# Kernel optimization log

Hardware: AMD Instinct MI355X
Metric: run time of the kernel (lower is better)

Reference implementation:

```python
import jax, jax.numpy as jnp
import numpy as np
import math

S, B, D, H = 2048, 4, 1024, 16
DH = D // H

def setup_inputs() -> dict:
    key = jax.random.key(0)
    ks = jax.random.split(key, 6)
    x = jax.random.normal(ks[0], (S, B, D), dtype=jnp.float32)
    # causal additive mask (finite large negative for numerical safety)
    i = jnp.arange(S)
    attn_mask = jnp.where(i[None, :] > i[:, None], jnp.float32(-1e9), jnp.float32(0.0))
    beta = jnp.zeros((H,), dtype=jnp.float32)  # per-head log-scale, init 0 -> exp=1
    xav = math.sqrt(6.0 / (D + D))  # xavier_uniform bound
    Wq = jax.random.uniform(ks[1], (D, D), minval=-xav, maxval=xav, dtype=jnp.float32)
    Wk = jax.random.uniform(ks[2], (D, D), minval=-xav, maxval=xav, dtype=jnp.float32)
    Wv = jax.random.uniform(ks[3], (D, D), minval=-xav, maxval=xav, dtype=jnp.float32)
    Wo = jax.random.uniform(ks[4], (D, D), minval=-xav, maxval=xav, dtype=jnp.float32)
    z = jnp.zeros((D,), dtype=jnp.float32)
    return {"x": x, "attn_mask": attn_mask, "beta": beta,
            "Wq": Wq, "bq": z, "Wk": Wk, "bk": z, "Wv": Wv, "bv": z, "Wo": Wo, "bo": z}

def reference(x, attn_mask, beta, Wq, bq, Wk, bk, Wv, bv, Wo, bo):
    s, b, d = x.shape
    h, dh = H, DH
    q = x @ Wq.T + bq  # (s, b, d)
    k = x @ Wk.T + bk
    v = x @ Wv.T + bv
    # attn_sink: append zero key/value token, pad mask with a zero column
    k = jnp.concatenate([k, jnp.zeros((1, b, d), k.dtype)], axis=0)  # (s+1, b, d)
    v = jnp.concatenate([v, jnp.zeros((1, b, d), v.dtype)], axis=0)
    mask = jnp.pad(attn_mask, ((0, 0), (0, 1)))  # (s, s+1)
    t = s + 1
    # split heads: (seq, b, h, dh) -> (b, h, seq, dh)
    qh = q.reshape(s, b, h, dh).transpose(1, 2, 0, 3)
    kh = k.reshape(t, b, h, dh).transpose(1, 2, 0, 3)
    vh = v.reshape(t, b, h, dh).transpose(1, 2, 0, 3)
    scale = (jnp.exp(beta) * math.sqrt(dh))[None, :, None, None]
    qh = qh / scale
    scores = jnp.einsum('bhsd,bhtd->bhst', qh, kh) + mask[None, None]
    w = jax.nn.softmax(scores, axis=-1)
    out = jnp.einsum('bhst,bhtd->bhsd', w, vh)  # (b, h, s, dh)
    out = out.transpose(2, 0, 1, 3).reshape(s, b, d)
    return out @ Wo.T + bo
```

## Files before the change

### kernel.cpp

```cpp
#include <hip/hip_runtime.h>
#include <hip/hip_bf16.h>
#include <math.h>

#define S_LEN   2048
#define BATCH   4
#define DMODEL  1024
#define NHEAD   16
#define DHEAD   64
#define MROWS   (S_LEN * BATCH)

typedef __bf16 bf16;
typedef __bf16 bf16x8 __attribute__((ext_vector_type(8)));
typedef __bf16 bf16x4 __attribute__((ext_vector_type(4)));
typedef short  short4_t __attribute__((ext_vector_type(4)));
typedef float  f32x4  __attribute__((ext_vector_type(4)));

#define LOG2E 1.4426950408889634f

#define AS1C(p) (const __attribute__((address_space(1))) void*)(p)
#define AS3(p)  (__attribute__((address_space(3))) void*)(p)


__global__ __launch_bounds__(256) void cast_bf16(const float* __restrict__ in,
                                                 bf16* __restrict__ out, int n8) {
    int i = blockIdx.x * 256 + threadIdx.x;
    if (i >= n8) return;
    const float4* p = (const float4*)in;
    float4 a = p[i * 2], b = p[i * 2 + 1];
    bf16x8 o;
    o[0] = (bf16)a.x; o[1] = (bf16)a.y; o[2] = (bf16)a.z; o[3] = (bf16)a.w;
    o[4] = (bf16)b.x; o[5] = (bf16)b.y; o[6] = (bf16)b.z; o[7] = (bf16)b.w;
    *(bf16x8*)(out + (size_t)i * 8) = o;
}

__global__ __launch_bounds__(256) void cast3_bf16(const float* __restrict__ w0,
                                                  const float* __restrict__ w1,
                                                  const float* __restrict__ w2,
                                                  bf16* __restrict__ out) {
    const int seg = blockIdx.y;
    const float* in = (seg == 0) ? w0 : (seg == 1) ? w1 : w2;
    int i = blockIdx.x * 256 + threadIdx.x;
    const float4* p = (const float4*)in;
    float4 a = p[i * 2], b = p[i * 2 + 1];
    bf16x8 o;
    o[0] = (bf16)a.x; o[1] = (bf16)a.y; o[2] = (bf16)a.z; o[3] = (bf16)a.w;
    o[4] = (bf16)b.x; o[5] = (bf16)b.y; o[6] = (bf16)b.z; o[7] = (bf16)b.w;
    *(bf16x8*)(out + (size_t)seg * DMODEL * DMODEL + (size_t)i * 8) = o;
}

__global__ __launch_bounds__(512, 4) void qkv_gemm(const bf16* __restrict__ A,
                                                   const bf16* __restrict__ W,
                                                   const float* __restrict__ bq,
                                                   const float* __restrict__ bk,
                                                   const float* __restrict__ bv,
                                                   const float* __restrict__ beta,
                                                   bf16* __restrict__ Qo,
                                                   bf16* __restrict__ Kp,
                                                   bf16* __restrict__ Vp) {
    constexpr int BK = 32;
    constexpr int NT = DMODEL / BK;
    __shared__ __align__(16) bf16 sA[3][256 * BK];
    __shared__ __align__(16) bf16 sB[3][128 * BK];
    const int t    = threadIdx.x;
    const int lane = t & 63;
    const int wave = t >> 6;
    const int wr   = wave >> 2;
    const int wc   = wave & 3;
    const int lq   = lane & 15;
    const int lg   = lane >> 4;
    const int bn   = blockIdx.x * 128;
    const int bm   = blockIdx.y * 256;

    const int schunk = (lane & 3) ^ ((lane >> 3) & 3);
    const bf16* ApS  = A + (size_t)(bm + wave * 32 + (lane >> 2)) * DMODEL + schunk * 8;
    const bf16* ApS2 = ApS + (size_t)16 * DMODEL;
    const bf16* WpS  = W + (size_t)(bn + wave * 16 + (lane >> 2)) * DMODEL + schunk * 8;
    const int koff = (lg ^ ((lq >> 1) & 3)) * 8;
    f32x4 acc[8][2] = {};

    __builtin_amdgcn_global_load_lds(AS1C(ApS),       AS3(&sA[0][wave*1024]),       16,0,0);
    __builtin_amdgcn_global_load_lds(AS1C(ApS2),      AS3(&sA[0][wave*1024 + 512]), 16,0,0);
    __builtin_amdgcn_global_load_lds(AS1C(WpS),       AS3(&sB[0][wave*512]),        16,0,0);
    __builtin_amdgcn_global_load_lds(AS1C(ApS  + BK), AS3(&sA[1][wave*1024]),       16,0,0);
    __builtin_amdgcn_global_load_lds(AS1C(ApS2 + BK), AS3(&sA[1][wave*1024 + 512]), 16,0,0);
    __builtin_amdgcn_global_load_lds(AS1C(WpS  + BK), AS3(&sB[1][wave*512]),        16,0,0);
    asm volatile("s_waitcnt vmcnt(3)\n\ts_barrier" ::: "memory");

    int bi = 0, si = 2, st = 2;
    for (int tt = 0; tt < NT; ++tt) {
        {
            const size_t ko = (size_t)st * BK;
            __builtin_amdgcn_global_load_lds(AS1C(ApS  + ko), AS3(&sA[si][wave*1024]),       16,0,0);
            __builtin_amdgcn_global_load_lds(AS1C(ApS2 + ko), AS3(&sA[si][wave*1024 + 512]), 16,0,0);
            __builtin_amdgcn_global_load_lds(AS1C(WpS  + ko), AS3(&sB[si][wave*512]),        16,0,0);
        }
        const bf16* At = sA[bi];
        const bf16* Bt = sB[bi];
        bf16x8 bf0 = *(const bf16x8*)&Bt[(wc*32 +      lq)*BK + koff];
        bf16x8 bf1 = *(const bf16x8*)&Bt[(wc*32 + 16 + lq)*BK + koff];
        bf16x8 af0[4];
#pragma unroll
        for (int mt = 0; mt < 4; mt++)
            af0[mt] = *(const bf16x8*)&At[(wr*128 + mt*16 + lq)*BK + koff];
        __builtin_amdgcn_s_setprio(1);
#pragma unroll
        for (int mt = 0; mt < 4; mt++) {
            acc[mt][0] = __builtin_amdgcn_mfma_f32_16x16x32_bf16(af0[mt], bf0, acc[mt][0],0,0,0);
            acc[mt][1] = __builtin_amdgcn_mfma_f32_16x16x32_bf16(af0[mt], bf1, acc[mt][1],0,0,0);
        }
        __builtin_amdgcn_s_setprio(0);
        bf16x8 af1[4];
#pragma unroll
        for (int mt = 0; mt < 4; mt++)
            af1[mt] = *(const bf16x8*)&At[(wr*128 + (mt+4)*16 + lq)*BK + koff];
        __builtin_amdgcn_s_setprio(1);
#pragma unroll
        for (int mt = 0; mt < 4; mt++) {
            acc[mt+4][0] = __builtin_amdgcn_mfma_f32_16x16x32_bf16(af1[mt], bf0, acc[mt+4][0],0,0,0);
            acc[mt+4][1] = __builtin_amdgcn_mfma_f32_16x16x32_bf16(af1[mt], bf1, acc[mt+4][1],0,0,0);
        }
        __builtin_amdgcn_s_setprio(0);
        asm volatile("s_waitcnt vmcnt(3)\n\ts_barrier" ::: "memory");
        bi = (bi == 2) ? 0 : bi + 1;
        si = (si == 2) ? 0 : si + 1;
        st = (st == NT - 1) ? 0 : st + 1;
    }

    const int seg = blockIdx.x >> 3;
    const int bnl = (blockIdx.x & 7) * 128;
    const float* bias = (seg == 0) ? bq : (seg == 1) ? bk : bv;

    if (seg == 0) {
#pragma unroll
        for (int nt = 0; nt < 2; nt++) {
            const int col = bnl + wc * 32 + nt * 16 + lq;
            const float bvv = bias[col];
            const float sc = LOG2E / (__expf(beta[col >> 6]) * 8.0f);
#pragma unroll
            for (int mt = 0; mt < 8; mt++) {
                const int row = bm + wr * 128 + mt * 16 + lg * 4;
#pragma unroll
                for (int r = 0; r < 4; r++) {
                    float v = (acc[mt][nt][r] + bvv) * sc;
                    Qo[(size_t)(row + r) * DMODEL + col] = (bf16)v;
                }
            }
        }
    } else {
        bf16* out = (seg == 1) ? Kp : Vp;
#pragma unroll
        for (int mt = 0; mt < 8; mt++) {
            const int F   = bm + wr * 128 + mt * 16;
            const int S0X = F >> 2;
            const int T   = S0X >> 4;
            const int sl  = (S0X & 15) + lg;
#pragma unroll
            for (int nt = 0; nt < 2; nt++) {
                const int col = bnl + wc * 32 + nt * 16 + lq;
                const int h   = col >> 6;
                const int dh  = col & 63;
                const float bvv = bias[col];
#pragma unroll
                for (int r = 0; r < 4; r++) {
                    float v = acc[mt][nt][r] + bvv;
                    size_t addr;
                    if (seg == 1) {
                        addr = ((size_t)((r * 16 + h) * 128 + T)) * 1024
                             + (dh >> 5) * 512
                             + (sl + 16 * ((dh >> 3) & 3)) * 8
                             + (dh & 7);
                    } else {
                        addr = ((size_t)((r * 16 + h) * 128 + T)) * 1024
                             + (dh >> 4) * 256 + ((dh & 15) + 16 * (sl >> 2)) * 4
                             + (sl & 3);
                    }
                    out[addr] = (bf16)v;
                }
            }
        }
    }
}

__global__ __launch_bounds__(256, 3) void gemm_out(const bf16* __restrict__ A,
                                                   const bf16* __restrict__ W,
                                                   const float* __restrict__ bias,
                                                   float* __restrict__ C) {
    constexpr int BK = 32;
    constexpr int NTILES = DMODEL / BK;
    __shared__ __align__(16) bf16 sA[3][128 * BK];
    __shared__ __align__(16) bf16 sB[3][128 * BK];

    const int t    = threadIdx.x;
    const int lane = t & 63;
    const int wave = t >> 6;
    const int wr   = wave >> 1;
    const int wc   = wave & 1;
    const int lq   = lane & 15;
    const int lg   = lane >> 4;
    const int bn   = blockIdx.x * 128;
    const int bm   = blockIdx.y * 128;

    const int schunk = (lane & 3) ^ ((lane >> 3) & 3);
    const bf16* ApS = A + (size_t)(bm + wave * 32 + (lane >> 2)) * DMODEL + schunk * 8;
    const bf16* WpS = W + (size_t)(bn + wave * 32 + (lane >> 2)) * DMODEL + schunk * 8;
    const int koff = (lg ^ ((lq >> 1) & 3)) * 8;

    f32x4 acc[4][4] = {};

#define OSTAGE(si_, ko_)                                                                              \
    __builtin_amdgcn_global_load_lds(AS1C(ApS + (ko_)),               AS3(&sA[si_][(wave*32 +  0)*BK]), 16,0,0); \
    __builtin_amdgcn_global_load_lds(AS1C(ApS + 16*DMODEL + (ko_)),   AS3(&sA[si_][(wave*32 + 16)*BK]), 16,0,0); \
    __builtin_amdgcn_global_load_lds(AS1C(WpS + (ko_)),               AS3(&sB[si_][(wave*32 +  0)*BK]), 16,0,0); \
    __builtin_amdgcn_global_load_lds(AS1C(WpS + 16*DMODEL + (ko_)),   AS3(&sB[si_][(wave*32 + 16)*BK]), 16,0,0);

    OSTAGE(0, 0)
    OSTAGE(1, BK)
    asm volatile("s_waitcnt vmcnt(4)\n\ts_barrier" ::: "memory");

    int bi = 0, si = 2, st = 2;
    for (int tt = 0; tt < NTILES; ++tt) {
        OSTAGE(si, (size_t)st * BK)
        const bf16* At = sA[bi];
        const bf16* Bt = sB[bi];
        bf16x8 bfr[4], af[4];
#pragma unroll
        for (int nt = 0; nt < 4; nt++)
            bfr[nt] = *(const bf16x8*)&Bt[(wc * 64 + nt * 16 + lq) * BK + koff];
#pragma unroll
        for (int mt = 0; mt < 4; mt++)
            af[mt] = *(const bf16x8*)&At[(wr * 64 + mt * 16 + lq) * BK + koff];
        __builtin_amdgcn_s_setprio(1);
#pragma unroll
        for (int mt = 0; mt < 4; mt++)
#pragma unroll
            for (int nt = 0; nt < 4; nt++)
                acc[mt][nt] = __builtin_amdgcn_mfma_f32_16x16x32_bf16(af[mt], bfr[nt], acc[mt][nt], 0, 0, 0);
        __builtin_amdgcn_s_setprio(0);
        asm volatile("s_waitcnt vmcnt(4)\n\ts_barrier" ::: "memory");
        bi = (bi == 2) ? 0 : bi + 1;
        si = (si == 2) ? 0 : si + 1;
        st = (st == NTILES - 1) ? 0 : st + 1;
    }
#undef OSTAGE

#pragma unroll
    for (int nt = 0; nt < 4; nt++) {
        const int col = bn + wc * 64 + nt * 16 + lq;
        const float bvv = bias[col];
#pragma unroll
        for (int mt = 0; mt < 4; mt++) {
            const int row = bm + wr * 64 + mt * 16 + lg * 4;
#pragma unroll
            for (int r = 0; r < 4; r++)
                C[(size_t)(row + r) * DMODEL + col] = acc[mt][nt][r] + bvv;
        }
    }
}

__global__ __launch_bounds__(256, 3) void attn_kernel(const bf16* __restrict__ Q,
                                                      const bf16* __restrict__ Kp,
                                                      const bf16* __restrict__ Vp,
                                                      bf16* __restrict__ O) {
    __shared__ __align__(16) float sO[64 * 65];
    __shared__ __align__(16) float sL[256];

    const int t    = threadIdx.x;
    const int lane = t & 63;
    const int wave = t >> 6;
    const int lq = lane & 15;
    const int lg = lane >> 4;

    const int bid = (int)blockIdx.x + 32 * ((int)blockIdx.y + 16 * (int)blockIdx.z);
    const int swz = (bid & 7) * 256 + (bid >> 3);
    const int qi  = 31 - (swz & 31);
    const int h   = (swz >> 5) & 15;
    const int b   = swz >> 9;
    const int qb  = qi * 64;

    bf16x8 qf[4][2];
#pragma unroll
    for (int nt = 0; nt < 4; nt++)
#pragma unroll
        for (int kc = 0; kc < 2; kc++)
            qf[nt][kc] = *(const bf16x8*)
                &Q[((size_t)(qb + nt * 16 + lq) * BATCH + b) * DMODEL + h * DHEAD + kc * 32 + lg * 8];

    f32x4 o_acc[4][4] = {};
    float l_lane[4] = {0.f, 0.f, 0.f, 0.f};

    const bf16* Kb = Kp + (size_t)(b * NHEAD + h) * 131072;
    const bf16* Vb = Vp + (size_t)(b * NHEAD + h) * 131072;

    bf16x8 kc0 = *(const bf16x8*)(Kb + (size_t)wave * 1024 + lane * 8);
    bf16x8 kc1 = *(const bf16x8*)(Kb + (size_t)wave * 1024 + 512 + lane * 8);
    bf16x4 vc0 = *(const bf16x4*)(Vb + (size_t)wave * 1024 +   0 + lane * 4);
    bf16x4 vc1 = *(const bf16x4*)(Vb + (size_t)wave * 1024 + 256 + lane * 4);
    bf16x4 vc2 = *(const bf16x4*)(Vb + (size_t)wave * 1024 + 512 + lane * 4);
    bf16x4 vc3 = *(const bf16x4*)(Vb + (size_t)wave * 1024 + 768 + lane * 4);

    for (int kt = 0; kt <= qi; kt++) {
        const int tn = ((kt < qi) ? (kt + 1) : 0) * 4 + wave;
        const bf16* Kn = Kb + (size_t)tn * 1024;
        const bf16* Vn = Vb + (size_t)tn * 1024;
        bf16x8 kn0 = *(const bf16x8*)(Kn + lane * 8);
        bf16x8 kn1 = *(const bf16x8*)(Kn + 512 + lane * 8);
        bf16x4 vn0 = *(const bf16x4*)(Vn +   0 + lane * 4);
        bf16x4 vn1 = *(const bf16x4*)(Vn + 256 + lane * 4);
        bf16x4 vn2 = *(const bf16x4*)(Vn + 512 + lane * 4);
        bf16x4 vn3 = *(const bf16x4*)(Vn + 768 + lane * 4);

        f32x4 st[4];
        __builtin_amdgcn_s_setprio(1);
#pragma unroll
        for (int nt = 0; nt < 4; nt++) {
            f32x4 a = {};
            a = __builtin_amdgcn_mfma_f32_16x16x32_bf16(kc0, qf[nt][0], a, 0, 0, 0);
            a = __builtin_amdgcn_mfma_f32_16x16x32_bf16(kc1, qf[nt][1], a, 0, 0, 0);
            st[nt] = a;
        }
        __builtin_amdgcn_s_setprio(0);

        if (kt == qi) {
#pragma unroll
            for (int nt = 0; nt < 4; nt++)
#pragma unroll
                for (int r = 0; r < 4; r++)
                    if (wave * 16 + lg * 4 + r > nt * 16 + lq) st[nt][r] = -1e30f;
        }

        short4_t pf[4];
#pragma unroll
        for (int nt = 0; nt < 4; nt++) {
            float p0 = __builtin_amdgcn_exp2f(st[nt][0]);
            float p1 = __builtin_amdgcn_exp2f(st[nt][1]);
            float p2 = __builtin_amdgcn_exp2f(st[nt][2]);
            float p3 = __builtin_amdgcn_exp2f(st[nt][3]);
            l_lane[nt] += (p0 + p1) + (p2 + p3);
            bf16x4 pv;
            pv[0] = (bf16)p0; pv[1] = (bf16)p1; pv[2] = (bf16)p2; pv[3] = (bf16)p3;
            pf[nt] = __builtin_bit_cast(short4_t, pv);
        }

        short4_t va0 = __builtin_bit_cast(short4_t, vc0);
        short4_t va1 = __builtin_bit_cast(short4_t, vc1);
        short4_t va2 = __builtin_bit_cast(short4_t, vc2);
        short4_t va3 = __builtin_bit_cast(short4_t, vc3);
        __builtin_amdgcn_s_setprio(1);
#pragma unroll
        for (int nt = 0; nt < 4; nt++) {
            o_acc[0][nt] = __builtin_amdgcn_mfma_f32_16x16x16bf16_1k(va0, pf[nt], o_acc[0][nt], 0, 0, 0);
            o_acc[1][nt] = __builtin_amdgcn_mfma_f32_16x16x16bf16_1k(va1, pf[nt], o_acc[1][nt], 0, 0, 0);
            o_acc[2][nt] = __builtin_amdgcn_mfma_f32_16x16x16bf16_1k(va2, pf[nt], o_acc[2][nt], 0, 0, 0);
            o_acc[3][nt] = __builtin_amdgcn_mfma_f32_16x16x16bf16_1k(va3, pf[nt], o_acc[3][nt], 0, 0, 0);
        }
        __builtin_amdgcn_s_setprio(0);

        kc0 = kn0; kc1 = kn1;
        vc0 = vn0; vc1 = vn1; vc2 = vn2; vc3 = vn3;
    }

#pragma unroll
    for (int nt = 0; nt < 4; nt++) {
        float v = l_lane[nt];
        v += __shfl_xor(v, 16);
        v += __shfl_xor(v, 32);
        if (lg == 0) sL[wave * 64 + nt * 16 + lq] = v;
    }

#pragma unroll
    for (int rd = 0; rd < 4; rd++) {
#pragma unroll
        for (int dtc = 0; dtc < 4; dtc++) {
            if (((wave + rd) & 3) == dtc) {
                if (rd == 0) {
#pragma unroll
                    for (int nt = 0; nt < 4; nt++)
#pragma unroll
                        for (int r = 0; r < 4; r++)
                            sO[(dtc * 16 + lg * 4 + r) * 65 + nt * 16 + lq] = o_acc[dtc][nt][r];
                } else {
#pragma unroll
                    for (int nt = 0; nt < 4; nt++)
#pragma unroll
                        for (int r = 0; r < 4; r++)
                            sO[(dtc * 16 + lg * 4 + r) * 65 + nt * 16 + lq] += o_acc[dtc][nt][r];
                }
            }
        }
        __syncthreads();
    }

    const int dt = wave;
    float rec[4];
#pragma unroll
    for (int nt = 0; nt < 4; nt++) {
        float lt = 1.0f + sL[nt * 16 + lq] + sL[64 + nt * 16 + lq]
                 + sL[128 + nt * 16 + lq] + sL[192 + nt * 16 + lq];
        rec[nt] = 1.0f / lt;
    }
#pragma unroll
    for (int nt = 0; nt < 4; nt++) {
        bf16x4 ov;
#pragma unroll
        for (int r = 0; r < 4; r++)
            ov[r] = (bf16)(sO[(dt * 16 + lg * 4 + r) * 65 + nt * 16 + lq] * rec[nt]);
        *(bf16x4*)&O[((size_t)(qb + nt * 16 + lq) * BATCH + b) * DMODEL + h * DHEAD + dt * 16 + lg * 4] = ov;
    }
}

extern "C" void kernel_launch(void* const* d_in, const int* in_sizes, int n_in,
                              void* d_out, int out_size, void* d_ws, size_t ws_size,
                              hipStream_t stream) {
    const float* x    = (const float*)d_in[0];
    const float* beta = (const float*)d_in[2];
    const float* Wq   = (const float*)d_in[3];
    const float* bq   = (const float*)d_in[4];
    const float* Wk   = (const float*)d_in[5];
    const float* bk   = (const float*)d_in[6];
    const float* Wv   = (const float*)d_in[7];
    const float* bv   = (const float*)d_in[8];
    const float* Wo   = (const float*)d_in[9];
    const float* bo   = (const float*)d_in[10];
    float* out = (float*)d_out;

    char* ws = (char*)d_ws;
    size_t off = 0;
    auto alloc = [&](size_t bytes) -> void* {
        void* p = ws + off;
        off += (bytes + 255) & ~(size_t)255;
        return p;
    };
    const size_t xbytes = (size_t)MROWS * DMODEL * sizeof(bf16);
    const size_t wbytes = (size_t)DMODEL * DMODEL * sizeof(bf16);
    bf16* xb   = (bf16*)alloc(xbytes);
    bf16* wqkv = (bf16*)alloc(3 * wbytes);
    bf16* wob  = (bf16*)alloc(wbytes);
    bf16* qws  = (bf16*)alloc(xbytes);
    bf16* kpb  = (bf16*)alloc(xbytes);
    bf16* vpb  = (bf16*)alloc(xbytes);
    bf16* aob  = (bf16*)alloc(xbytes);

    const int nx8 = MROWS * DMODEL / 8;
    const int nw8 = DMODEL * DMODEL / 8;
    cast_bf16<<<(nx8 + 255) / 256, 256, 0, stream>>>(x, xb, nx8);
    cast_bf16<<<(nw8 + 255) / 256, 256, 0, stream>>>(Wo, wob, nw8);
    dim3 c3grid(nw8 / 256, 3);
    cast3_bf16<<<c3grid, 256, 0, stream>>>(Wq, Wk, Wv, wqkv);

    dim3 qgrid(3 * DMODEL / 128, MROWS / 256);
    qkv_gemm<<<qgrid, 512, 0, stream>>>(xb, wqkv, bq, bk, bv, beta, qws, kpb, vpb);

    dim3 agrid(S_LEN / 64, NHEAD, BATCH);
    attn_kernel<<<agrid, 256, 0, stream>>>(qws, kpb, vpb, aob);

    dim3 ogrid(DMODEL / 128, MROWS / 128);
    gemm_out<<<ogrid, 256, 0, stream>>>(aob, wob, bo, out);
}
```

Baseline: 281.7 us.

## Pair causal query tiles per attention block and merge cast kernels

The attention kernel now launches half as many blocks, and each block handles two query tiles (qi and 31-qi). Every block therefore does the same amount of causal work, which balances load and removes the tail from uneven block lengths. Separately, the three fp32-to-bf16 cast launches are folded into a single kernel that selects its source and destination by index. The risk is fewer, longer blocks with two serial passes, which could reduce overlap and occupancy.

```diff
diff --git a/kernel.cpp b/kernel.cpp
--- a/kernel.cpp
+++ b/kernel.cpp
@@ -21,31 +21,37 @@
 #define AS3(p)  (__attribute__((address_space(3))) void*)(p)
 
 
-__global__ __launch_bounds__(256) void cast_bf16(const float* __restrict__ in,
-                                                 bf16* __restrict__ out, int n8) {
-    int i = blockIdx.x * 256 + threadIdx.x;
-    if (i >= n8) return;
-    const float4* p = (const float4*)in;
-    float4 a = p[i * 2], b = p[i * 2 + 1];
+__global__ __launch_bounds__(256) void cast_all(const float* __restrict__ x,
+                                                const float* __restrict__ wq,
+                                                const float* __restrict__ wk,
+                                                const float* __restrict__ wv,
+                                                const float* __restrict__ wo,
+                                                bf16* __restrict__ xb,
+                                                bf16* __restrict__ wqkv,
+                                                bf16* __restrict__ wob) {
+    const int i = blockIdx.x * 256 + threadIdx.x;
+    constexpr int NX8 = MROWS * DMODEL / 8;
+    constexpr int NW8 = DMODEL * DMODEL / 8;
+    const float* src;
+    bf16* dst;
+    int k;
+    if (i < NX8) {
+        src = x; dst = xb; k = i;
+    } else {
+        const int j   = i - NX8;
+        const int seg = j >> 17;
+        k = j & (NW8 - 1);
+        if (seg == 0)      { src = wq; dst = wqkv; }
+        else if (seg == 1) { src = wk; dst = wqkv + (size_t)DMODEL * DMODEL; }
+        else if (seg == 2) { src = wv; dst = wqkv + (size_t)2 * DMODEL * DMODEL; }
+        else               { src = wo; dst = wob; }
+    }
+    const float4* p = (const float4*)src;
+    float4 a = p[(size_t)k * 2], b = p[(size_t)k * 2 + 1];
     bf16x8 o;
     o[0] = (bf16)a.x; o[1] = (bf16)a.y; o[2] = (bf16)a.z; o[3] = (bf16)a.w;
     o[4] = (bf16)b.x; o[5] = (bf16)b.y; o[6] = (bf16)b.z; o[7] = (bf16)b.w;
-    *(bf16x8*)(out + (size_t)i * 8) = o;
-}
-
-__global__ __launch_bounds__(256) void cast3_bf16(const float* __restrict__ w0,
-                                                  const float* __restrict__ w1,
-                                                  const float* __restrict__ w2,
-                                                  bf16* __restrict__ out) {
-    const int seg = blockIdx.y;
-    const float* in = (seg == 0) ? w0 : (seg == 1) ? w1 : w2;
-    int i = blockIdx.x * 256 + threadIdx.x;
-    const float4* p = (const float4*)in;
-    float4 a = p[i * 2], b = p[i * 2 + 1];
-    bf16x8 o;
-    o[0] = (bf16)a.x; o[1] = (bf16)a.y; o[2] = (bf16)a.z; o[3] = (bf16)a.w;
-    o[4] = (bf16)b.x; o[5] = (bf16)b.y; o[6] = (bf16)b.z; o[7] = (bf16)b.w;
-    *(bf16x8*)(out + (size_t)seg * DMODEL * DMODEL + (size_t)i * 8) = o;
+    *(bf16x8*)(dst + (size_t)k * 8) = o;
 }
 
 __global__ __launch_bounds__(512, 4) void qkv_gemm(const bf16* __restrict__ A,
@@ -270,141 +276,148 @@
     const int lq = lane & 15;
     const int lg = lane >> 4;
 
-    const int bid = (int)blockIdx.x + 32 * ((int)blockIdx.y + 16 * (int)blockIdx.z);
-    const int swz = (bid & 7) * 256 + (bid >> 3);
-    const int qi  = 31 - (swz & 31);
-    const int h   = (swz >> 5) & 15;
-    const int b   = swz >> 9;
-    const int qb  = qi * 64;
-
-    bf16x8 qf[4][2];
-#pragma unroll
-    for (int nt = 0; nt < 4; nt++)
-#pragma unroll
-        for (int kc = 0; kc < 2; kc++)
-            qf[nt][kc] = *(const bf16x8*)
-                &Q[((size_t)(qb + nt * 16 + lq) * BATCH + b) * DMODEL + h * DHEAD + kc * 32 + lg * 8];
-
-    f32x4 o_acc[4][4] = {};
-    float l_lane[4] = {0.f, 0.f, 0.f, 0.f};
+    const int bid = (int)blockIdx.x + 16 * ((int)blockIdx.y + 16 * (int)blockIdx.z);
+    const int swz = (bid & 7) * 128 + (bid >> 3);
+    const int idx = swz & 15;
+    const int h   = (swz >> 4) & 15;
+    const int b   = swz >> 8;
 
     const bf16* Kb = Kp + (size_t)(b * NHEAD + h) * 131072;
     const bf16* Vb = Vp + (size_t)(b * NHEAD + h) * 131072;
 
-    bf16x8 kc0 = *(const bf16x8*)(Kb + (size_t)wave * 1024 + lane * 8);
-    bf16x8 kc1 = *(const bf16x8*)(Kb + (size_t)wave * 1024 + 512 + lane * 8);
-    bf16x4 vc0 = *(const bf16x4*)(Vb + (size_t)wave * 1024 +   0 + lane * 4);
-    bf16x4 vc1 = *(const bf16x4*)(Vb + (size_t)wave * 1024 + 256 + lane * 4);
-    bf16x4 vc2 = *(const bf16x4*)(Vb + (size_t)wave * 1024 + 512 + lane * 4);
-    bf16x4 vc3 = *(const bf16x4*)(Vb + (size_t)wave * 1024 + 768 + lane * 4);
-
-    for (int kt = 0; kt <= qi; kt++) {
-        const int tn = ((kt < qi) ? (kt + 1) : 0) * 4 + wave;
-        const bf16* Kn = Kb + (size_t)tn * 1024;
-        const bf16* Vn = Vb + (size_t)tn * 1024;
-        bf16x8 kn0 = *(const bf16x8*)(Kn + lane * 8);
-        bf16x8 kn1 = *(const bf16x8*)(Kn + 512 + lane * 8);
-        bf16x4 vn0 = *(const bf16x4*)(Vn +   0 + lane * 4);
-        bf16x4 vn1 = *(const bf16x4*)(Vn + 256 + lane * 4);
-        bf16x4 vn2 = *(const bf16x4*)(Vn + 512 + lane * 4);
-        bf16x4 vn3 = *(const bf16x4*)(Vn + 768 + lane * 4);
-
-        f32x4 st[4];
-        __builtin_amdgcn_s_setprio(1);
+#pragma clang loop unroll(disable)
+    for (int pass = 0; pass < 2; ++pass) {
+        const int qi = (pass == 0) ? (31 - idx) : idx;
+        const int qb = qi * 64;
+
+        bf16x8 qf[4][2];
+#pragma unroll
+        for (int nt = 0; nt < 4; nt++)
+#pragma unroll
+            for (int kc = 0; kc < 2; kc++)
+                qf[nt][kc] = *(const bf16x8*)
+                    &Q[((size_t)(qb + nt * 16 + lq) * BATCH + b) * DMODEL + h * DHEAD + kc * 32 + lg * 8];
+
+        f32x4 o_acc[4][4] = {};
+        float l_lane[4] = {0.f, 0.f, 0.f, 0.f};
+
+        bf16x8 kc0 = *(const bf16x8*)(Kb + (size_t)wave * 1024 + lane * 8);
+        bf16x8 kc1 = *(const bf16x8*)(Kb + (size_t)wave * 1024 + 512 + lane * 8);
+        bf16x4 vc0 = *(const bf16x4*)(Vb + (size_t)wave * 1024 +   0 + lane * 4);
+        bf16x4 vc1 = *(const bf16x4*)(Vb + (size_t)wave * 1024 + 256 + lane * 4);
+        bf16x4 vc2 = *(const bf16x4*)(Vb + (size_t)wave * 1024 + 512 + lane * 4);
+        bf16x4 vc3 = *(const bf16x4*)(Vb + (size_t)wave * 1024 + 768 + lane * 4);
+
+        for (int kt = 0; kt <= qi; kt++) {
+            const int tn = ((kt < qi) ? (kt + 1) : 0) * 4 + wave;
+            const bf16* Kn = Kb + (size_t)tn * 1024;
+            const bf16* Vn = Vb + (size_t)tn * 1024;
+            bf16x8 kn0 = *(const bf16x8*)(Kn + lane * 8);
+            bf16x8 kn1 = *(const bf16x8*)(Kn + 512 + lane * 8);
+            bf16x4 vn0 = *(const bf16x4*)(Vn +   0 + lane * 4);
+            bf16x4 vn1 = *(const bf16x4*)(Vn + 256 + lane * 4);
+            bf16x4 vn2 = *(const bf16x4*)(Vn + 512 + lane * 4);
+            bf16x4 vn3 = *(const bf16x4*)(Vn + 768 + lane * 4);
+
+            f32x4 st[4];
+            __builtin_amdgcn_s_setprio(1);
+#pragma unroll
+            for (int nt = 0; nt < 4; nt++) {
+                f32x4 a = {};
+                a = __builtin_amdgcn_mfma_f32_16x16x32_bf16(kc0, qf[nt][0], a, 0, 0, 0);
+                a = __builtin_amdgcn_mfma_f32_16x16x32_bf16(kc1, qf[nt][1], a, 0, 0, 0);
+                st[nt] = a;
+            }
+            __builtin_amdgcn_s_setprio(0);
+
+            if (kt == qi) {
+#pragma unroll
+                for (int nt = 0; nt < 4; nt++)
+#pragma unroll
+                    for (int r = 0; r < 4; r++)
+                        if (wave * 16 + lg * 4 + r > nt * 16 + lq) st[nt][r] = -1e30f;
+            }
+
+            short4_t pf[4];
+#pragma unroll
+            for (int nt = 0; nt < 4; nt++) {
+                float p0 = __builtin_amdgcn_exp2f(st[nt][0]);
+                float p1 = __builtin_amdgcn_exp2f(st[nt][1]);
+                float p2 = __builtin_amdgcn_exp2f(st[nt][2]);
+                float p3 = __builtin_amdgcn_exp2f(st[nt][3]);
+                l_lane[nt] += (p0 + p1) + (p2 + p3);
+                bf16x4 pv;
+                pv[0] = (bf16)p0; pv[1] = (bf16)p1; pv[2] = (bf16)p2; pv[3] = (bf16)p3;
+                pf[nt] = __builtin_bit_cast(short4_t, pv);
+            }
+
+            short4_t va0 = __builtin_bit_cast(short4_t, vc0);
+            short4_t va1 = __builtin_bit_cast(short4_t, vc1);
+            short4_t va2 = __builtin_bit_cast(short4_t, vc2);
+            short4_t va3 = __builtin_bit_cast(short4_t, vc3);
+            __builtin_amdgcn_s_setprio(1);
+#pragma unroll
+            for (int nt = 0; nt < 4; nt++) {
+                o_acc[0][nt] = __builtin_amdgcn_mfma_f32_16x16x16bf16_1k(va0, pf[nt], o_acc[0][nt], 0, 0, 0);
+                o_acc[1][nt] = __builtin_amdgcn_mfma_f32_16x16x16bf16_1k(va1, pf[nt], o_acc[1][nt], 0, 0, 0);
+                o_acc[2][nt] = __builtin_amdgcn_mfma_f32_16x16x16bf16_1k(va2, pf[nt], o_acc[2][nt], 0, 0, 0);
+                o_acc[3][nt] = __builtin_amdgcn_mfma_f32_16x16x16bf16_1k(va3, pf[nt], o_acc[3][nt], 0, 0, 0);
+            }
+            __builtin_amdgcn_s_setprio(0);
+
+            kc0 = kn0; kc1 = kn1;
+            vc0 = vn0; vc1 = vn1; vc2 = vn2; vc3 = vn3;
+        }
+
 #pragma unroll
         for (int nt = 0; nt < 4; nt++) {
-            f32x4 a = {};
-            a = __builtin_amdgcn_mfma_f32_16x16x32_bf16(kc0, qf[nt][0], a, 0, 0, 0);
-            a = __builtin_amdgcn_mfma_f32_16x16x32_bf16(kc1, qf[nt][1], a, 0, 0, 0);
-            st[nt] = a;
-        }
-        __builtin_amdgcn_s_setprio(0);
-
-        if (kt == qi) {
-#pragma unroll
-            for (int nt = 0; nt < 4; nt++)
-#pragma unroll
-                for (int r = 0; r < 4; r++)
-                    if (wave * 16 + lg * 4 + r > nt * 16 + lq) st[nt][r] = -1e30f;
-        }
-
-        short4_t pf[4];
+            float v = l_lane[nt];
+            v += __shfl_xor(v, 16);
+            v += __shfl_xor(v, 32);
+            if (lg == 0) sL[wave * 64 + nt * 16 + lq] = v;
+        }
+
+#pragma unroll
+        for (int rd = 0; rd < 4; rd++) {
+#pragma unroll
+            for (int dtc = 0; dtc < 4; dtc++) {
+                if (((wave + rd) & 3) == dtc) {
+                    if (rd == 0) {
+#pragma unroll
+                        for (int nt = 0; nt < 4; nt++)
+#pragma unroll
+                            for (int r = 0; r < 4; r++)
+                                sO[(dtc * 16 + lg * 4 + r) * 65 + nt * 16 + lq] = o_acc[dtc][nt][r];
+                    } else {
+#pragma unroll
+                        for (int nt = 0; nt < 4; nt++)
+#pragma unroll
+                            for (int r = 0; r < 4; r++)
+                                sO[(dtc * 16 + lg * 4 + r) * 65 + nt * 16 + lq] += o_acc[dtc][nt][r];
+                    }
+                }
+            }
+            __syncthreads();
+        }
+
+        const int dt = wave;
+        float rec[4];
 #pragma unroll
         for (int nt = 0; nt < 4; nt++) {
-            float p0 = __builtin_amdgcn_exp2f(st[nt][0]);
-            float p1 = __builtin_amdgcn_exp2f(st[nt][1]);
-            float p2 = __builtin_amdgcn_exp2f(st[nt][2]);
-            float p3 = __builtin_amdgcn_exp2f(st[nt][3]);
-            l_lane[nt] += (p0 + p1) + (p2 + p3);
-            bf16x4 pv;
-            pv[0] = (bf16)p0; pv[1] = (bf16)p1; pv[2] = (bf16)p2; pv[3] = (bf16)p3;
-            pf[nt] = __builtin_bit_cast(short4_t, pv);
-        }
-
-        short4_t va0 = __builtin_bit_cast(short4_t, vc0);
-        short4_t va1 = __builtin_bit_cast(short4_t, vc1);
-        short4_t va2 = __builtin_bit_cast(short4_t, vc2);
-        short4_t va3 = __builtin_bit_cast(short4_t, vc3);
-        __builtin_amdgcn_s_setprio(1);
+            float lt = 1.0f + sL[nt * 16 + lq] + sL[64 + nt * 16 + lq]
+                     + sL[128 + nt * 16 + lq] + sL[192 + nt * 16 + lq];
+            rec[nt] = 1.0f / lt;
+        }
 #pragma unroll
         for (int nt = 0; nt < 4; nt++) {
-            o_acc[0][nt] = __builtin_amdgcn_mfma_f32_16x16x16bf16_1k(va0, pf[nt], o_acc[0][nt], 0, 0, 0);
-            o_acc[1][nt] = __builtin_amdgcn_mfma_f32_16x16x16bf16_1k(va1, pf[nt], o_acc[1][nt], 0, 0, 0);
-            o_acc[2][nt] = __builtin_amdgcn_mfma_f32_16x16x16bf16_1k(va2, pf[nt], o_acc[2][nt], 0, 0, 0);
-            o_acc[3][nt] = __builtin_amdgcn_mfma_f32_16x16x16bf16_1k(va3, pf[nt], o_acc[3][nt], 0, 0, 0);
-        }
-        __builtin_amdgcn_s_setprio(0);
-
-        kc0 = kn0; kc1 = kn1;
-        vc0 = vn0; vc1 = vn1; vc2 = vn2; vc3 = vn3;
-    }
-
-#pragma unroll
-    for (int nt = 0; nt < 4; nt++) {
-        float v = l_lane[nt];
-        v += __shfl_xor(v, 16);
-        v += __shfl_xor(v, 32);
-        if (lg == 0) sL[wave * 64 + nt * 16 + lq] = v;
-    }
-
-#pragma unroll
-    for (int rd = 0; rd < 4; rd++) {
-#pragma unroll
-        for (int dtc = 0; dtc < 4; dtc++) {
-            if (((wave + rd) & 3) == dtc) {
-                if (rd == 0) {
-#pragma unroll
-                    for (int nt = 0; nt < 4; nt++)
-#pragma unroll
-                        for (int r = 0; r < 4; r++)
-                            sO[(dtc * 16 + lg * 4 + r) * 65 + nt * 16 + lq] = o_acc[dtc][nt][r];
-                } else {
-#pragma unroll
-                    for (int nt = 0; nt < 4; nt++)
-#pragma unroll
-                        for (int r = 0; r < 4; r++)
-                            sO[(dtc * 16 + lg * 4 + r) * 65 + nt * 16 + lq] += o_acc[dtc][nt][r];
-                }
-            }
-        }
+            bf16x4 ov;
+#pragma unroll
+            for (int r = 0; r < 4; r++)
+                ov[r] = (bf16)(sO[(dt * 16 + lg * 4 + r) * 65 + nt * 16 + lq] * rec[nt]);
+            *(bf16x4*)&O[((size_t)(qb + nt * 16 + lq) * BATCH + b) * DMODEL + h * DHEAD + dt * 16 + lg * 4] = ov;
+        }
+
         __syncthreads();
-    }
-
-    const int dt = wave;
-    float rec[4];
-#pragma unroll
-    for (int nt = 0; nt < 4; nt++) {
-        float lt = 1.0f + sL[nt * 16 + lq] + sL[64 + nt * 16 + lq]
-                 + sL[128 + nt * 16 + lq] + sL[192 + nt * 16 + lq];
-        rec[nt] = 1.0f / lt;
-    }
-#pragma unroll
-    for (int nt = 0; nt < 4; nt++) {
-        bf16x4 ov;
-#pragma unroll
-        for (int r = 0; r < 4; r++)
-            ov[r] = (bf16)(sO[(dt * 16 + lg * 4 + r) * 65 + nt * 16 + lq] * rec[nt]);
-        *(bf16x4*)&O[((size_t)(qb + nt * 16 + lq) * BATCH + b) * DMODEL + h * DHEAD + dt * 16 + lg * 4] = ov;
     }
 }
 
@@ -440,17 +453,14 @@
     bf16* vpb  = (bf16*)alloc(xbytes);
     bf16* aob  = (bf16*)alloc(xbytes);
 
-    const int nx8 = MROWS * DMODEL / 8;
-    const int nw8 = DMODEL * DMODEL / 8;
-    cast_bf16<<<(nx8 + 255) / 256, 256, 0, stream>>>(x, xb, nx8);
-    cast_bf16<<<(nw8 + 255) / 256, 256, 0, stream>>>(Wo, wob, nw8);
-    dim3 c3grid(nw8 / 256, 3);
-    cast3_bf16<<<c3grid, 256, 0, stream>>>(Wq, Wk, Wv, wqkv);
+    constexpr int NX8 = MROWS * DMODEL / 8;
+    constexpr int NW8 = DMODEL * DMODEL / 8;
+    cast_all<<<(NX8 + 4 * NW8) / 256, 256, 0, stream>>>(x, Wq, Wk, Wv, Wo, xb, wqkv, wob);
 
     dim3 qgrid(3 * DMODEL / 128, MROWS / 256);
     qkv_gemm<<<qgrid, 512, 0, stream>>>(xb, wqkv, bq, bk, bv, beta, qws, kpb, vpb);
 
-    dim3 agrid(S_LEN / 64, NHEAD, BATCH);
+    dim3 agrid(S_LEN / 128, NHEAD, BATCH);
     attn_kernel<<<agrid, 256, 0, stream>>>(qws, kpb, vpb, aob);
 
     dim3 ogrid(DMODEL / 128, MROWS / 128);
```

After: 277.7 us. Within noise of the previous version (-1.4%).
